# Kernel optimization log

Measured on AMD Instinct MI355X. Metric: run time of the kernel, lower is better.

Reference implementation:

```python
import jax, jax.numpy as jnp
import numpy as np

N_HEADS = 16

def setup_inputs() -> dict:
    key = jax.random.key(0)
    kx, kk, kq, kv, ko = jax.random.split(key, 5)
    B, T, D = 8, 1024, 1024
    s = 1.0 / np.sqrt(D)
    return {
        'x':  jax.random.normal(kx, (B, T, D), dtype=jnp.float32),
        'Wk': jax.random.normal(kk, (D, D), dtype=jnp.float32) * s,
        'Wq': jax.random.normal(kq, (D, D), dtype=jnp.float32) * s,
        'Wv': jax.random.normal(kv, (D, D), dtype=jnp.float32) * s,
        'Wo': jax.random.normal(ko, (D, D), dtype=jnp.float32) * s,
    }

def reference(x, Wk, Wq, Wv, Wo):
    B, T, D = x.shape
    H = D // N_HEADS  # head dim
    # projections (nn.Linear with bias=False: y = x @ W^T)
    k = (x @ Wk.T).reshape(B, T, N_HEADS, H).transpose(0, 2, 1, 3)  # [B,n,T,H]
    q = (x @ Wq.T).reshape(B, T, N_HEADS, H).transpose(0, 2, 1, 3)
    v = (x @ Wv.T).reshape(B, T, N_HEADS, H).transpose(0, 2, 1, 3)
    scores = jnp.einsum('bnqh,bnkh->bnqk', q, k)                    # [B,n,T,T]
    causal = jnp.tril(jnp.ones((T, T), dtype=bool))
    # original: masked_fill(-inf) BEFORE scaling; -inf/sqrt(H) stays -inf
    scores = jnp.where(causal, scores, -jnp.inf) / jnp.sqrt(jnp.float32(H))
    att = jax.nn.softmax(scores, axis=-1)
    # dropout p=0.0 -> identity
    out = jnp.einsum('bnqk,bnkh->bnqh', att, v)                     # [B,n,T,H]
    out = out.transpose(0, 2, 1, 3).reshape(B, T, D)
    return out @ Wo.T
```

## Files before the change

### kernel.cpp

```cpp
#include <hip/hip_runtime.h>
#include <stdint.h>

typedef __bf16 bf16x8 __attribute__((ext_vector_type(8)));
typedef float f32x4 __attribute__((ext_vector_type(4)));
typedef unsigned short ushort_t;
typedef unsigned int uint_t;

__device__ inline ushort_t f2bf(float f) {
  uint_t u = __builtin_bit_cast(uint_t, f);
  u = (u + 0x7FFFu + ((u >> 16) & 1u)) >> 16;
  return (ushort_t)u;
}

__device__ inline void gll16(const void* g, void* l) {
  __builtin_amdgcn_global_load_lds(
      (__attribute__((address_space(1))) void*)(uintptr_t)g,
      (__attribute__((address_space(3))) void*)(uint32_t)(uintptr_t)l,
      16, 0, 0);
}

__global__ void cast_bf16(const float* __restrict__ in, ushort_t* __restrict__ out,
                          int n4, float scale) {
  int i = blockIdx.x * blockDim.x + threadIdx.x;
  int st = gridDim.x * blockDim.x;
  for (; i < n4; i += st) {
    float4 v = reinterpret_cast<const float4*>(in)[i];
    ushort4 o;
    o.x = f2bf(v.x * scale);
    o.y = f2bf(v.y * scale);
    o.z = f2bf(v.z * scale);
    o.w = f2bf(v.w * scale);
    reinterpret_cast<ushort4*>(out)[i] = o;
  }
}

__global__ void cast_w4(const float* __restrict__ w0, const float* __restrict__ w1,
                        const float* __restrict__ w2, const float* __restrict__ w3,
                        ushort_t* __restrict__ out, float s0) {
  const int i = blockIdx.x * 256 + threadIdx.x;
  const int which = i >> 18;
  const float* src = which == 0 ? w0 : which == 1 ? w1 : which == 2 ? w2 : w3;
  const float sc = which == 0 ? s0 : 1.0f;
  float4 v = reinterpret_cast<const float4*>(src)[i & 0x3FFFF];
  ushort4 o;
  o.x = f2bf(v.x * sc);
  o.y = f2bf(v.y * sc);
  o.z = f2bf(v.z * sc);
  o.w = f2bf(v.w * sc);
  reinterpret_cast<ushort4*>(out)[i] = o;
}

#define MFMA16(A_, B_, C_) __builtin_amdgcn_mfma_f32_16x16x32_bf16(A_, B_, C_, 0, 0, 0)
#define SBAR __builtin_amdgcn_s_barrier
#define LGKM0 asm volatile("s_waitcnt lgkmcnt(0)" ::: "memory")

template <int MF, int NF, int NTN, int LDC, bool F32OUT>
__global__ __launch_bounds__(512, 2) void gemm8p(const ushort_t* __restrict__ A,
                                                 const ushort_t* __restrict__ B,
                                                 void* __restrict__ C) {
  constexpr int BM = MF * 32;
  constexpr int BN = NF * 64;
  constexpr int NA = BM / 64;
  constexpr int NB = BN / 64;
  constexpr int NB0 = (NB >= 2) ? NB / 2 : 1;
  constexpr int NG0 = (NF >= 2) ? NF / 2 : 1;
  constexpr int AU = BM * 64;
  constexpr int BUF = AU + BN * 64;
  constexpr int NWG = (8192 / BM) * NTN;
  __shared__ __attribute__((aligned(16))) ushort_t smem[2 * BUF];

  const int tid = threadIdx.x;
  const int lane = tid & 63;
  const int w = tid >> 6;
  const int wm = w >> 2, wn = w & 3;

  const int bid = blockIdx.x;
  const int swz = (bid & 7) * (NWG / 8) + (bid >> 3);
  const int m0 = (swz / NTN) * BM;
  const int n0 = (swz % NTN) * BN;

  const int scol = ((tid & 7) ^ ((tid >> 3) & 7)) * 8;
  const ushort_t* gA = A + (size_t)(m0 + (tid >> 3)) * 1024 + scol;
  const ushort_t* gB = B + (size_t)(n0 + (tid >> 3)) * 1024 + scol;

  const int lr = lane & 15;
  const int hi = lane >> 4;
  const int arow = (wm * MF * 16 + lr) * 64;
  const int brow = AU + (wn * NF * 16 + lr) * 64;
  const int cx0 = (hi * 8) ^ ((lane & 7) << 3);
  const int cx1 = cx0 ^ 32;

  f32x4 acc[MF][NF] = {};
  bf16x8 a[MF / 2][2];
  bf16x8 b[NF][2];

  auto stage_a_even = [&](int wbu, int sk) __attribute__((always_inline)) {
    if constexpr (MF == 8) {
      gll16(gA + 0 * 65536 + sk, &smem[wbu + 0 * 4096 + (w << 9)]);
      gll16(gA + 2 * 65536 + sk, &smem[wbu + 2 * 4096 + (w << 9)]);
    } else {
#pragma unroll
      for (int i = 0; i < NA; ++i)
        gll16(gA + i * 65536 + sk, &smem[wbu + i * 4096 + (w << 9)]);
    }
  };
  auto stage_a_odd = [&](int wbu, int sk) __attribute__((always_inline)) {
    if constexpr (MF == 8) {
      gll16(gA + 1 * 65536 + sk, &smem[wbu + 1 * 4096 + (w << 9)]);
      gll16(gA + 3 * 65536 + sk, &smem[wbu + 3 * 4096 + (w << 9)]);
    }
  };
  auto stage_b0 = [&](int wbu, int sk) __attribute__((always_inline)) {
#pragma unroll
    for (int i = 0; i < NB0; ++i)
      gll16(gB + i * 65536 + sk, &smem[wbu + AU + i * 4096 + (w << 9)]);
  };
  auto stage_b1 = [&](int wbu, int sk) __attribute__((always_inline)) {
#pragma unroll
    for (int i = NB0; i < NB; ++i)
      gll16(gB + i * 65536 + sk, &smem[wbu + AU + i * 4096 + (w << 9)]);
  };
  auto rdA = [&](int rbu, int mbase) __attribute__((always_inline)) {
#pragma unroll
    for (int m = 0; m < MF / 2; ++m) {
      const int base = rbu + arow + (mbase + m) * 1024;
      a[m][0] = *(const bf16x8*)&smem[base + cx0];
      a[m][1] = *(const bf16x8*)&smem[base + cx1];
    }
  };
  auto rdBg = [&](int rbu, int ng0, int ng1) __attribute__((always_inline)) {
#pragma unroll
    for (int n = 0; n < NF; ++n) {
      if (n < ng0 || n >= ng1) continue;
      const int base = rbu + brow + n * 1024;
      b[n][0] = *(const bf16x8*)&smem[base + cx0];
      b[n][1] = *(const bf16x8*)&smem[base + cx1];
    }
  };
  auto mmg = [&](int mbase, int ng0, int ng1) __attribute__((always_inline)) {
#pragma unroll
    for (int m = 0; m < MF / 2; ++m)
#pragma unroll
      for (int n = 0; n < NF; ++n) {
        if (n < ng0 || n >= ng1) continue;
        acc[mbase + m][n] = MFMA16(a[m][0], b[n][0], acc[mbase + m][n]);
        acc[mbase + m][n] = MFMA16(a[m][1], b[n][1], acc[mbase + m][n]);
      }
  };

  auto tile = [&](int rbu, int wbu, int sk, bool pf) __attribute__((always_inline)) {
    if (pf) {
      stage_a_even(wbu, sk);
      if constexpr (MF == 8)
        asm volatile("s_waitcnt vmcnt(4)" ::: "memory");
      else
        asm volatile("s_waitcnt vmcnt(2)" ::: "memory");
    } else {
      if constexpr (MF == 8)
        asm volatile("s_waitcnt vmcnt(2)" ::: "memory");
      else
        asm volatile("s_waitcnt vmcnt(0)" ::: "memory");
    }
    SBAR();
    rdA(rbu, 0);
    rdBg(rbu, 0, NG0);
    LGKM0;
    __builtin_amdgcn_s_setprio(1);
    mmg(0, 0, NG0);
    __builtin_amdgcn_s_setprio(0);
    SBAR();
    rdBg(rbu, NG0, NF);
    if (pf) stage_b0(wbu, sk);
    SBAR();
    LGKM0;
    __builtin_amdgcn_s_setprio(1);
    mmg(0, NG0, NF);
    __builtin_amdgcn_s_setprio(0);
    SBAR();
    if (pf) {
      stage_b1(wbu, sk);
      if constexpr (MF == 8)
        asm volatile("s_waitcnt vmcnt(5)" ::: "memory");
    } else {
      if constexpr (MF == 8)
        asm volatile("s_waitcnt vmcnt(0)" ::: "memory");
    }
    SBAR();
    rdA(rbu, MF / 2);
    LGKM0;
    __builtin_amdgcn_s_setprio(1);
    mmg(MF / 2, NG0, NF);
    __builtin_amdgcn_s_setprio(0);
    SBAR();
    if (pf) stage_a_odd(wbu, sk);
    SBAR();
    __builtin_amdgcn_s_setprio(1);
    mmg(MF / 2, 0, NG0);
    __builtin_amdgcn_s_setprio(0);
    SBAR();
  };

  stage_a_even(0, 0);
  stage_b0(0, 0);
  stage_b1(0, 0);
  stage_a_odd(0, 0);
  int sk = 64;
  for (int it = 0; it < 7; ++it) {
    tile(0, BUF, sk, true);
    sk += 64;
    tile(BUF, 0, sk, true);
    sk += 64;
  }
  tile(0, BUF, sk, true);
  tile(BUF, 0, 0, false);

  const size_t erow = (size_t)(m0 + wm * MF * 16 + hi * 4);
  const int ecol = n0 + wn * NF * 16 + lr;
#pragma unroll
  for (int mf = 0; mf < MF; ++mf)
#pragma unroll
    for (int nf = 0; nf < NF; ++nf)
#pragma unroll
      for (int r = 0; r < 4; ++r) {
        const size_t idx = (erow + mf * 16 + r) * LDC + ecol + nf * 16;
        if constexpr (F32OUT)
          ((float*)C)[idx] = acc[mf][nf][r];
        else
          ((ushort_t*)C)[idx] = f2bf(acc[mf][nf][r]);
      }
}

__global__ __launch_bounds__(256, 2) void attn_fwd(const ushort_t* __restrict__ QKV,
                                                   ushort_t* __restrict__ ctx) {
  const int bid = blockIdx.x;
  const int h = bid & 15;
  const int b = (bid >> 4) & 7;
  const int p = bid >> 7;
  const int tid = threadIdx.x;
  const int lane = tid & 63;
  const int w = tid >> 6;
  const int lr = lane & 15;
  const int lg = lane >> 4;
  const int dk = lg << 3;

  __shared__ __attribute__((aligned(16))) ushort_t Ks[2][64 * 72];
  __shared__ __attribute__((aligned(16))) uint_t VtDw[2][64 * 36];
  __shared__ __attribute__((aligned(16))) ushort_t Pl[4][32 * 72];

  const int kkey = tid >> 2, kdg = tid & 3;
  const int vkp = tid & 31, vdg = tid >> 5;
  const ushort_t* kgbase =
      QKV + ((size_t)(b * 1024 + kkey)) * 3072 + 1024 + h * 64 + kdg * 16;
  const ushort_t* vgbase =
      QKV + ((size_t)(b * 1024 + 2 * vkp)) * 3072 + 2048 + h * 64 + vdg * 8;

  const float FMAX2 = 23.083120654223414f;

  const int qtA = p, qtB = 7 - p;
  const int ntB = (qtB + 1) << 1;
  const int wrow0A = (qtA << 7) + w * 32;
  const int wrow0B = (qtB << 7) + w * 32;

  bf16x8 qfA[2][2], qfB[2][2];
#pragma unroll
  for (int i = 0; i < 2; ++i) {
    const ushort_t* qpA =
        QKV + ((size_t)(b * 1024 + wrow0A + i * 16 + lr)) * 3072 + h * 64 + dk;
    qfA[i][0] = *reinterpret_cast<const bf16x8*>(qpA);
    qfA[i][1] = *reinterpret_cast<const bf16x8*>(qpA + 32);
    const ushort_t* qpB =
        QKV + ((size_t)(b * 1024 + wrow0B + i * 16 + lr)) * 3072 + h * 64 + dk;
    qfB[i][0] = *reinterpret_cast<const bf16x8*>(qpB);
    qfB[i][1] = *reinterpret_cast<const bf16x8*>(qpB + 32);
  }

  f32x4 oA[2][4] = {}, oB[2][4] = {};
  float lsA[2] = {0.f, 0.f}, lsB[2] = {0.f, 0.f};

  uint4 rk0 = *reinterpret_cast<const uint4*>(kgbase);
  uint4 rk1 = *reinterpret_cast<const uint4*>(kgbase + 8);
  uint4 rv0 = *reinterpret_cast<const uint4*>(vgbase);
  uint4 rv1 = *reinterpret_cast<const uint4*>(vgbase + 3072);

  for (int t = 0; t < ntB; ++t) {
    const int bsel = t & 1;
    asm volatile("s_waitcnt vmcnt(0)" ::: "memory");
    {
      uint_t* kd = reinterpret_cast<uint_t*>(&Ks[bsel][kkey * 72 + kdg * 16]);
      *reinterpret_cast<uint4*>(kd) = rk0;
      *reinterpret_cast<uint4*>(kd + 4) = rk1;
      const ushort_t* e0 = reinterpret_cast<const ushort_t*>(&rv0);
      const ushort_t* e1 = reinterpret_cast<const ushort_t*>(&rv1);
#pragma unroll
      for (int j = 0; j < 8; ++j)
        VtDw[bsel][(vdg * 8 + j) * 36 + vkp] = (uint_t)e0[j] | ((uint_t)e1[j] << 16);
    }
    if (t + 1 < ntB) {
      const size_t off = (size_t)(t + 1) * 64 * 3072;
      rk0 = *reinterpret_cast<const uint4*>(kgbase + off);
      rk1 = *reinterpret_cast<const uint4*>(kgbase + off + 8);
      rv0 = *reinterpret_cast<const uint4*>(vgbase + off);
      rv1 = *reinterpret_cast<const uint4*>(vgbase + off + 3072);
    }
    asm volatile("s_waitcnt lgkmcnt(0)" ::: "memory");
    __builtin_amdgcn_s_barrier();

    const int kb = t << 6;
    const bool actB = (kb <= wrow0B + 31);
    const bool actA = (kb <= wrow0A + 31);
    if (!(actA || actB)) continue;

    bf16x8 kf0[4], kf1[4];
#pragma unroll
    for (int f = 0; f < 4; ++f) {
      kf0[f] = *reinterpret_cast<const bf16x8*>(&Ks[bsel][(f * 16 + lr) * 72 + dk]);
      kf1[f] =
          *reinterpret_cast<const bf16x8*>(&Ks[bsel][(f * 16 + lr) * 72 + 32 + dk]);
    }
    bf16x8 vb[2][4];
#pragma unroll
    for (int kblk = 0; kblk < 2; ++kblk)
#pragma unroll
      for (int fh = 0; fh < 4; ++fh)
        vb[kblk][fh] = *reinterpret_cast<const bf16x8*>(
            &VtDw[bsel][(fh * 16 + lr) * 36 + kblk * 16 + (lg << 2)]);

    auto group = [&](const bf16x8(&qf)[2][2], f32x4(&o)[2][4], float(&ls)[2],
                     int wrow0) __attribute__((always_inline)) {
      f32x4 s[2][4];
#pragma unroll
      for (int i = 0; i < 2; ++i)
#pragma unroll
        for (int f = 0; f < 4; ++f) {
          f32x4 z = {0.f, 0.f, 0.f, 0.f};
          z = __builtin_amdgcn_mfma_f32_16x16x32_bf16(kf0[f], qf[i][0], z, 0, 0, 0);
          s[i][f] = __builtin_amdgcn_mfma_f32_16x16x32_bf16(kf1[f], qf[i][1], z, 0, 0, 0);
        }
      const bool needmask = (kb + 63 > wrow0);
#pragma unroll
      for (int i = 0; i < 2; ++i) {
        const int qr = wrow0 + i * 16 + lr;
#pragma unroll
        for (int f = 0; f < 4; ++f) {
          const int kbase = kb + f * 16 + (lg << 2);
          float p0 = __builtin_amdgcn_exp2f(s[i][f][0] - FMAX2);
          float p1 = __builtin_amdgcn_exp2f(s[i][f][1] - FMAX2);
          float p2 = __builtin_amdgcn_exp2f(s[i][f][2] - FMAX2);
          float p3 = __builtin_amdgcn_exp2f(s[i][f][3] - FMAX2);
          if (needmask) {
            p0 = (kbase + 0 <= qr) ? p0 : 0.f;
            p1 = (kbase + 1 <= qr) ? p1 : 0.f;
            p2 = (kbase + 2 <= qr) ? p2 : 0.f;
            p3 = (kbase + 3 <= qr) ? p3 : 0.f;
          }
          ls[i] += (p0 + p1) + (p2 + p3);
          uint_t q01, q23;
          asm("v_cvt_pk_bf16_f32 %0, %1, %2" : "=v"(q01) : "v"(p0), "v"(p1));
          asm("v_cvt_pk_bf16_f32 %0, %1, %2" : "=v"(q23) : "v"(p2), "v"(p3));
          uint2 pk = {q01, q23};
          *reinterpret_cast<uint2*>(
              &Pl[w][(i * 16 + lr) * 72 + f * 16 + (lg << 2)]) = pk;
        }
      }
#pragma unroll
      for (int i = 0; i < 2; ++i)
#pragma unroll
        for (int kblk = 0; kblk < 2; ++kblk) {
          const bf16x8 pa = *reinterpret_cast<const bf16x8*>(
              &Pl[w][(i * 16 + lr) * 72 + kblk * 32 + dk]);
#pragma unroll
          for (int fh = 0; fh < 4; ++fh)
            o[i][fh] = __builtin_amdgcn_mfma_f32_16x16x32_bf16(pa, vb[kblk][fh],
                                                               o[i][fh], 0, 0, 0);
        }
    };

    if (actB) group(qfB, oB, lsB, wrow0B);
    if (actA) group(qfA, oA, lsA, wrow0A);
  }

  auto epi = [&](f32x4(&o)[2][4], float(&ls)[2], int wrow0)
      __attribute__((always_inline)) {
#pragma unroll
    for (int i = 0; i < 2; ++i) {
      float s = ls[i];
      s += __shfl_xor(s, 16);
      s += __shfl_xor(s, 32);
      const float linv = 1.0f / s;
      const size_t crow = (size_t)(b * 1024 + wrow0 + i * 16 + (lg << 2));
#pragma unroll
      for (int r = 0; r < 4; ++r) {
        const float li = __shfl(linv, (lg << 2) + r);
#pragma unroll
        for (int fh = 0; fh < 4; ++fh)
          ctx[(crow + r) * 1024 + h * 64 + fh * 16 + lr] = f2bf(o[i][fh][r] * li);
      }
    }
  };
  epi(oB, lsB, wrow0B);
  epi(oA, lsA, wrow0A);
}

extern "C" void kernel_launch(void* const* d_in, const int* in_sizes, int n_in,
                              void* d_out, int out_size, void* d_ws, size_t ws_size,
                              hipStream_t stream) {
  const float* x = (const float*)d_in[0];
  const float* Wk = (const float*)d_in[1];
  const float* Wq = (const float*)d_in[2];
  const float* Wv = (const float*)d_in[3];
  const float* Wo = (const float*)d_in[4];

  char* ws = (char*)d_ws;
  ushort_t* xb = (ushort_t*)ws;
  ushort_t* Wc = (ushort_t*)(ws + (16u << 20));
  ushort_t* Wob = Wc + 3u * 1024 * 1024;
  ushort_t* QKV = (ushort_t*)(ws + (24u << 20));
  ushort_t* ctx = xb;

  cast_bf16<<<2048, 256, 0, stream>>>(x, xb, (8192 * 1024) / 4, 1.0f);
  cast_w4<<<4096, 256, 0, stream>>>(Wq, Wk, Wv, Wo, Wc, 0.125f * 1.4426950408889634f);

  gemm8p<4, 2, 24, 3072, false><<<1536, 512, 0, stream>>>(xb, Wc, QKV);

  attn_fwd<<<512, 256, 0, stream>>>(QKV, ctx);

  gemm8p<4, 2, 8, 1024, true><<<512, 512, 0, stream>>>(ctx, Wob, (float*)d_out);
}
```

Baseline: 132.2 us.

## Merge cast kernels, retile QKV GEMM, and raise MFMA wave priority in attention

Result: faster. 129.2 us (-2.2%).

```diff
diff --git a/kernel.cpp b/kernel.cpp
--- a/kernel.cpp
+++ b/kernel.cpp
@@ -19,35 +19,34 @@
       16, 0, 0);
 }
 
-__global__ void cast_bf16(const float* __restrict__ in, ushort_t* __restrict__ out,
-                          int n4, float scale) {
-  int i = blockIdx.x * blockDim.x + threadIdx.x;
-  int st = gridDim.x * blockDim.x;
-  for (; i < n4; i += st) {
-    float4 v = reinterpret_cast<const float4*>(in)[i];
-    ushort4 o;
-    o.x = f2bf(v.x * scale);
-    o.y = f2bf(v.y * scale);
-    o.z = f2bf(v.z * scale);
-    o.w = f2bf(v.w * scale);
-    reinterpret_cast<ushort4*>(out)[i] = o;
+__global__ void cast_all(const float* __restrict__ x, const float* __restrict__ w0,
+                         const float* __restrict__ w1, const float* __restrict__ w2,
+                         const float* __restrict__ w3, ushort_t* __restrict__ xb,
+                         ushort_t* __restrict__ wc, float s0) {
+  const int i = blockIdx.x * 256 + threadIdx.x;
+  const float* src;
+  ushort_t* dst;
+  float sc = 1.0f;
+  int j;
+  if (i < (1 << 21)) {
+    src = x;
+    dst = xb;
+    j = i;
+  } else {
+    const int k = i - (1 << 21);
+    const int which = k >> 18;
+    src = which == 0 ? w0 : which == 1 ? w1 : which == 2 ? w2 : w3;
+    if (which == 0) sc = s0;
+    dst = wc + (k >> 18) * (1 << 20);
+    j = k & 0x3FFFF;
   }
-}
-
-__global__ void cast_w4(const float* __restrict__ w0, const float* __restrict__ w1,
-                        const float* __restrict__ w2, const float* __restrict__ w3,
-                        ushort_t* __restrict__ out, float s0) {
-  const int i = blockIdx.x * 256 + threadIdx.x;
-  const int which = i >> 18;
-  const float* src = which == 0 ? w0 : which == 1 ? w1 : which == 2 ? w2 : w3;
-  const float sc = which == 0 ? s0 : 1.0f;
-  float4 v = reinterpret_cast<const float4*>(src)[i & 0x3FFFF];
+  float4 v = reinterpret_cast<const float4*>(src)[j];
   ushort4 o;
   o.x = f2bf(v.x * sc);
   o.y = f2bf(v.y * sc);
   o.z = f2bf(v.z * sc);
   o.w = f2bf(v.w * sc);
-  reinterpret_cast<ushort4*>(out)[i] = o;
+  reinterpret_cast<ushort4*>(dst)[j] = o;
 }
 
 #define MFMA16(A_, B_, C_) __builtin_amdgcn_mfma_f32_16x16x32_bf16(A_, B_, C_, 0, 0, 0)
@@ -328,6 +327,7 @@
     auto group = [&](const bf16x8(&qf)[2][2], f32x4(&o)[2][4], float(&ls)[2],
                      int wrow0) __attribute__((always_inline)) {
       f32x4 s[2][4];
+      __builtin_amdgcn_s_setprio(1);
 #pragma unroll
       for (int i = 0; i < 2; ++i)
 #pragma unroll
@@ -336,6 +336,7 @@
           z = __builtin_amdgcn_mfma_f32_16x16x32_bf16(kf0[f], qf[i][0], z, 0, 0, 0);
           s[i][f] = __builtin_amdgcn_mfma_f32_16x16x32_bf16(kf1[f], qf[i][1], z, 0, 0, 0);
         }
+      __builtin_amdgcn_s_setprio(0);
       const bool needmask = (kb + 63 > wrow0);
 #pragma unroll
       for (int i = 0; i < 2; ++i) {
@@ -362,6 +363,7 @@
               &Pl[w][(i * 16 + lr) * 72 + f * 16 + (lg << 2)]) = pk;
         }
       }
+      __builtin_amdgcn_s_setprio(1);
 #pragma unroll
       for (int i = 0; i < 2; ++i)
 #pragma unroll
@@ -373,6 +375,7 @@
             o[i][fh] = __builtin_amdgcn_mfma_f32_16x16x32_bf16(pa, vb[kblk][fh],
                                                                o[i][fh], 0, 0, 0);
         }
+      __builtin_amdgcn_s_setprio(0);
     };
 
     if (actB) group(qfB, oB, lsB, wrow0B);
@@ -417,10 +420,10 @@
   ushort_t* QKV = (ushort_t*)(ws + (24u << 20));
   ushort_t* ctx = xb;
 
-  cast_bf16<<<2048, 256, 0, stream>>>(x, xb, (8192 * 1024) / 4, 1.0f);
-  cast_w4<<<4096, 256, 0, stream>>>(Wq, Wk, Wv, Wo, Wc, 0.125f * 1.4426950408889634f);
-
-  gemm8p<4, 2, 24, 3072, false><<<1536, 512, 0, stream>>>(xb, Wc, QKV);
+  cast_all<<<12288, 256, 0, stream>>>(x, Wq, Wk, Wv, Wo, xb, Wc,
+                                      0.125f * 1.4426950408889634f);
+
+  gemm8p<8, 3, 16, 3072, false><<<512, 512, 0, stream>>>(xb, Wc, QKV);
 
   attn_fwd<<<512, 256, 0, stream>>>(QKV, ctx);
 
```
